# Kernel optimization log

Measured on AMD Instinct MI355X. Metric: run time of the kernel, lower is better.

## Reference

```python
import jax, jax.numpy as jnp
import numpy as np

HEADS = 8
DIM_HEAD = 64
C = 512              # in_channels == inner_dim = heads*dim_head
WIN = 7              # window size implied by rel_pos table (2*7-1 = 13)
EPS = 1e-5


def setup_inputs() -> dict:
    key = jax.random.key(0)
    ks = jax.random.split(key, 6)
    B = 2048
    inner = HEADS * DIM_HEAD
    x = jax.random.normal(ks[0], (B, C, WIN, WIN), dtype=jnp.float32)
    gamma = jnp.ones((C,), dtype=jnp.float32)
    beta = jnp.zeros((C,), dtype=jnp.float32)
    w_qkv = jax.random.normal(ks[1], (C, 3 * inner), dtype=jnp.float32) / np.sqrt(C)
    rel_table = jax.random.normal(ks[2], (2 * WIN - 1, 2 * WIN - 1, HEADS), dtype=jnp.float32)
    w_out = jax.random.normal(ks[3], (inner, C), dtype=jnp.float32) / np.sqrt(inner)
    b_out = jnp.zeros((C,), dtype=jnp.float32)
    return {"x": x, "gamma": gamma, "beta": beta, "w_qkv": w_qkv,
            "rel_table": rel_table, "w_out": w_out, "b_out": b_out}


def _rel_pos_bias(rel_table, H, W):
    # Swin-style additive bias: bias[h, i, j] = table[hi-hj+H-1, wi-wj+W-1, h]
    hh = jnp.arange(H)
    ww = jnp.arange(W)
    hi = jnp.repeat(hh, W)          # [N] row index of each flattened position
    wi = jnp.tile(ww, H)            # [N] col index
    dh = hi[:, None] - hi[None, :] + (H - 1)   # [N, N]
    dw = wi[:, None] - wi[None, :] + (W - 1)   # [N, N]
    bias = rel_table[dh, dw]        # [N, N, heads]
    return jnp.transpose(bias, (2, 0, 1))      # [heads, N, N]


def reference(x, gamma, beta, w_qkv, rel_table, w_out, b_out):
    B, Cc, H, W = x.shape
    N = H * W
    shortcut = x
    xs = jnp.transpose(x.reshape(B, Cc, N), (0, 2, 1))   # [B, N, C]
    # LayerNorm over channel dim
    mu = jnp.mean(xs, axis=-1, keepdims=True)
    var = jnp.var(xs, axis=-1, keepdims=True)
    xn = (xs - mu) * jax.lax.rsqrt(var + EPS) * gamma + beta
    qkv = xn @ w_qkv                                      # [B, N, 3*inner]
    q, k, v = jnp.split(qkv, 3, axis=-1)
    def heads(t):
        return jnp.transpose(t.reshape(B, N, HEADS, DIM_HEAD), (0, 2, 1, 3))  # [B,h,N,d]
    q, k, v = heads(q), heads(k), heads(v)
    scale = DIM_HEAD ** -0.5
    dots = jnp.einsum('bhnd,bhmd->bhnm', q, k) * scale   # [B,h,N,N]
    dots = dots + _rel_pos_bias(rel_table, H, W)[None]   # add Swin-style bias
    attn = jax.nn.softmax(dots, axis=-1)
    out = jnp.einsum('bhnm,bhmd->bhnd', attn, v)         # [B,h,N,d]
    out = jnp.transpose(out, (0, 2, 1, 3)).reshape(B, N, HEADS * DIM_HEAD)
    out = out @ w_out + b_out                            # [B, N, C]
    out = jnp.transpose(out, (0, 2, 1)).reshape(B, Cc, H, W)
    return out + shortcut
```

## Files before the change

kernel.cpp:

```cpp
#include <hip/hip_runtime.h>

#define BATCH 2048
#define CH 512
#define NTOK 49
#define NHEAD 8
#define DHEAD 64

typedef __attribute__((ext_vector_type(8))) short bf16x8;
typedef __attribute__((ext_vector_type(4))) float f32x4;

__device__ __forceinline__ ushort f2bf(float f) {
  union { float f; unsigned u; } v; v.f = f;
  unsigned r = v.u + 0x7fffu + ((v.u >> 16) & 1u);
  return (ushort)(r >> 16);
}

#define MFMA16(a, b, c) __builtin_amdgcn_mfma_f32_16x16x32_bf16((a), (b), (c), 0, 0, 0)

#define GLOAD_LDS16(gsrc, ldst)                                                  \
  __builtin_amdgcn_global_load_lds((const __attribute__((address_space(1))) void*)(gsrc), \
                                   (__attribute__((address_space(3))) void*)(ldst), 16, 0, 0)

__global__ void prep_kernel(const float* __restrict__ w_qkv, const float* __restrict__ w_out,
                            const float* __restrict__ rel, ushort* __restrict__ wqkvB,
                            ushort* __restrict__ woutF, float* __restrict__ biasP) {
  int tid = blockIdx.x * blockDim.x + threadIdx.x;
  int stride = gridDim.x * blockDim.x;
  for (int i = tid; i < 12 * 16 * 8 * 64 * 8; i += stride) {
    int j = i & 7, lane = (i >> 3) & 63, cbs = (i >> 9) & 7, kk = (i >> 12) & 15, nb = i >> 16;
    int o = nb * 128 + cbs * 16 + (lane & 15);
    int c = kk * 32 + (lane >> 4) * 8 + j;
    wqkvB[i] = f2bf(w_qkv[c * 1536 + o]);
  }
  for (int i = tid; i < 32 * 16 * 64 * 8; i += stride) {
    int j = i & 7, lane = (i >> 3) & 63, ks = (i >> 9) & 15, cb = i >> 13;
    int o = cb * 16 + (lane & 15);
    int c = ks * 32 + (lane >> 4) * 8 + j;
    woutF[i] = f2bf(w_out[c * 512 + o]);
  }
  for (int i = tid; i < NHEAD * 64 * 64; i += stride) {
    int h = i >> 12, n = (i >> 6) & 63, m = i & 63;
    float v = -1e30f;
    if (n < NTOK && m < NTOK) {
      int dh = n / 7 - m / 7 + 6;
      int dw = n % 7 - m % 7 + 6;
      v = rel[(dh * 13 + dw) * 8 + h];
    }
    biasP[i] = v;
  }
}

__global__ __launch_bounds__(256) void ln_kernel(const float* __restrict__ x,
                                                 const float* __restrict__ gamma,
                                                 const float* __restrict__ beta,
                                                 ushort* __restrict__ xnW) {
  int b = blockIdx.x;
  int t = threadIdx.x;
  __shared__ float xs[128][51];
  __shared__ float muL[64], rsL[64];
  const float* xb = x + (size_t)b * CH * NTOK;
  int row = t >> 2, sub = t & 3;
  float s = 0.f, s2 = 0.f;
  for (int cc = 0; cc < 4; cc++) {
    const float4* src4 = (const float4*)(xb + cc * 128 * NTOK);
    for (int i4 = t; i4 < 1568; i4 += 256) {
      float4 v = src4[i4];
      int lf = i4 * 4;
#pragma unroll
      for (int e = 0; e < 4; e++) {
        int c = (lf + e) / NTOK, n = (lf + e) - c * NTOK;
        xs[c][n] = ((const float*)&v)[e];
      }
    }
    __syncthreads();
    if (row < NTOK) {
      for (int c = sub; c < 128; c += 4) {
        float v = xs[c][row];
        s += v;
        s2 += v * v;
      }
    }
    __syncthreads();
  }
  s += __shfl_xor(s, 1);
  s += __shfl_xor(s, 2);
  s2 += __shfl_xor(s2, 1);
  s2 += __shfl_xor(s2, 2);
  if (sub == 0 && row < NTOK) {
    float m = s * (1.f / CH);
    muL[row] = m;
    rsL[row] = rsqrtf(s2 * (1.f / CH) - m * m + 1e-5f);
  }
  __syncthreads();
  ushort* dst = xnW + (size_t)b * NTOK * CH;
  for (int cc = 0; cc < 4; cc++) {
    const float4* src4 = (const float4*)(xb + cc * 128 * NTOK);
    for (int i4 = t; i4 < 1568; i4 += 256) {
      float4 v = src4[i4];
      int lf = i4 * 4;
#pragma unroll
      for (int e = 0; e < 4; e++) {
        int c = (lf + e) / NTOK, n = (lf + e) - c * NTOK;
        xs[c][n] = ((const float*)&v)[e];
      }
    }
    __syncthreads();
    for (int i = t; i < NTOK * 16; i += 256) {
      int n = i >> 4, c0 = (i & 15) * 8;
      ushort tmp[8];
#pragma unroll
      for (int j = 0; j < 8; j++) {
        int c = cc * 128 + c0 + j;
        tmp[j] = f2bf((xs[c0 + j][n] - muL[n]) * rsL[n] * gamma[c] + beta[c]);
      }
      *(uint4*)(dst + (size_t)n * CH + cc * 128 + c0) = *(const uint4*)tmp;
    }
    __syncthreads();
  }
}

__global__ __launch_bounds__(256, 4) void qkv_gemm(const ushort* __restrict__ xnW,
                                                   const ushort* __restrict__ wqkvB,
                                                   ushort* __restrict__ qW,
                                                   ushort* __restrict__ kW,
                                                   ushort* __restrict__ vW) {
  int bid = blockIdx.x;
  int f = (bid & 7) * 1536 + (bid >> 3);
  int mb = f / 12, nb = f - mb * 12;
  int b0 = mb * 2;
  int t = threadIdx.x, lane = t & 63, w = t >> 6;
  int wm = w >> 1, wn = w & 1;

  __shared__ __align__(16) ushort lds[16384];

  for (int i = t; i < 2 * 30 * 32; i += 256) {
    int buf = i >= 960;
    int r2 = i - buf * 960;
    int rr = r2 >> 5;
    int row = (rr < 15) ? (49 + rr) : (98 + rr);
    lds[buf * 8192 + row * 32 + (i & 31)] = 0;
  }

  const int arow = lane & 15, g = lane >> 4;
  int srow0 = w * 16 + (lane >> 2);
  int cL = lane & 3;
  const ushort* wBbase = wqkvB + (size_t)nb * 16 * 4096;

  {
#pragma unroll
    for (int i = 0; i < 2; i++) {
      int row = i * 64 + srow0;
      int n = row & 63, bb = b0 + (row >> 6);
      int cG = cL ^ ((row >> 1) & 3);
      if (n < NTOK)
        GLOAD_LDS16(xnW + ((size_t)bb * NTOK + n) * CH + cG * 8, lds + (i * 64 + w * 16) * 32);
    }
    GLOAD_LDS16(wBbase + (w * 2 + 0) * 512 + lane * 8, lds + 4096 + (w * 2 + 0) * 512);
    GLOAD_LDS16(wBbase + (w * 2 + 1) * 512 + lane * 8, lds + 4096 + (w * 2 + 1) * 512);
  }
  __syncthreads();

  f32x4 acc[4][4];
#pragma unroll
  for (int mt = 0; mt < 4; mt++)
#pragma unroll
    for (int nt = 0; nt < 4; nt++) acc[mt][nt] = (f32x4){0.f, 0.f, 0.f, 0.f};

  int cur = 0;
  for (int step = 0; step < 16; ++step) {
    if (step < 15) {
      int nxt = cur ^ 1, kk = step + 1;
#pragma unroll
      for (int i = 0; i < 2; i++) {
        int row = i * 64 + srow0;
        int n = row & 63, bb = b0 + (row >> 6);
        int cG = cL ^ ((row >> 1) & 3);
        if (n < NTOK)
          GLOAD_LDS16(xnW + ((size_t)bb * NTOK + n) * CH + kk * 32 + cG * 8,
                      lds + nxt * 8192 + (i * 64 + w * 16) * 32);
      }
      const ushort* wp = wBbase + (size_t)kk * 4096;
      GLOAD_LDS16(wp + (w * 2 + 0) * 512 + lane * 8, lds + nxt * 8192 + 4096 + (w * 2 + 0) * 512);
      GLOAD_LDS16(wp + (w * 2 + 1) * 512 + lane * 8, lds + nxt * 8192 + 4096 + (w * 2 + 1) * 512);
    }
    const ushort* lA = lds + cur * 8192;
    const ushort* lB = lds + cur * 8192 + 4096;
    bf16x8 bfr[4], afr[4];
#pragma unroll
    for (int nt = 0; nt < 4; nt++)
      bfr[nt] = *(const bf16x8*)&lB[((wn * 4 + nt) * 64 + lane) * 8];
#pragma unroll
    for (int mt = 0; mt < 4; mt++) {
      int row = wm * 64 + mt * 16 + arow;
      afr[mt] = *(const bf16x8*)&lA[row * 32 + (g ^ ((row >> 1) & 3)) * 8];
    }
#pragma unroll
    for (int mt = 0; mt < 4; mt++)
#pragma unroll
      for (int nt = 0; nt < 4; nt++) acc[mt][nt] = MFMA16(afr[mt], bfr[nt], acc[mt][nt]);
    __syncthreads();
    cur ^= 1;
  }

  ushort(*oL)[136] = (ushort(*)[136])lds;
  int h0 = (nb & 3) * 2;
  int sct = nb >> 2;
#pragma unroll
  for (int hh = 0; hh < 2; hh++) {
    if (wm == hh) {
#pragma unroll
      for (int mt = 0; mt < 4; mt++)
#pragma unroll
        for (int nt = 0; nt < 4; nt++)
#pragma unroll
          for (int r = 0; r < 4; r++) {
            int rn = mt * 16 + 4 * g + r;
            oL[rn][wn * 64 + nt * 16 + arow] = f2bf(acc[mt][nt][r]);
          }
    }
    __syncthreads();
    int b = b0 + hh;
    if (sct < 2) {
      ushort* dst = (sct == 0 ? qW : kW);
      for (int i = t; i < NTOK * 16; i += 256) {
        int n = i >> 4, c8 = i & 15;
        int h = h0 + (c8 >> 3);
        *(uint4*)(dst + (size_t)(b * 8 + h) * (NTOK * 64) + n * 64 + (c8 & 7) * 8) =
            *(const uint4*)&oL[n][c8 * 8];
      }
    } else {
      for (int i = t; i < 128 * 8; i += 256) {
        int col = i >> 3, n8 = i & 7;
        int h = h0 + (col >> 6), d = col & 63;
        ushort tmp[8];
#pragma unroll
        for (int jj = 0; jj < 8; jj++) tmp[jj] = oL[n8 * 8 + jj][col];
        *(uint4*)(vW + (size_t)(b * 8 + h) * 4096 + d * 64 + n8 * 8) = *(const uint4*)tmp;
      }
    }
    __syncthreads();
  }
}

__global__ __launch_bounds__(512, 4) void attn2(const ushort* __restrict__ qW,
                                                const ushort* __restrict__ kW,
                                                const ushort* __restrict__ vW,
                                                const float* __restrict__ biasP,
                                                ushort* __restrict__ aoW) {
  int b = blockIdx.x;
  int t = threadIdx.x;
  int lane = t & 63;
  int h = t >> 6;

  __shared__ ushort pL[8][64][72];
  ushort(*pl)[72] = pL[h];

  const int c = lane & 15, g = lane >> 4;
  const ushort* qb = qW + (size_t)(b * 8 + h) * NTOK * 64;
  const ushort* kb = kW + (size_t)(b * 8 + h) * NTOK * 64;
  const ushort* vb = vW + (size_t)(b * 8 + h) * 64 * 64;
  const float* bp = biasP + h * 64 * 64;

  f32x4 s[4][4];
#pragma unroll
  for (int mt = 0; mt < 4; mt++)
#pragma unroll
    for (int nt = 0; nt < 4; nt++) s[mt][nt] = (f32x4){0.f, 0.f, 0.f, 0.f};
#pragma unroll
  for (int ks = 0; ks < 2; ks++) {
    bf16x8 kf[4];
#pragma unroll
    for (int nt = 0; nt < 4; nt++)
      kf[nt] = *(const bf16x8*)(kb + (size_t)(nt * 16 + c) * 64 + ks * 32 + g * 8);
#pragma unroll
    for (int mt = 0; mt < 4; mt++) {
      bf16x8 qf = *(const bf16x8*)(qb + (size_t)(mt * 16 + c) * 64 + ks * 32 + g * 8);
#pragma unroll
      for (int nt = 0; nt < 4; nt++) s[mt][nt] = MFMA16(qf, kf[nt], s[mt][nt]);
    }
  }
#pragma unroll
  for (int mt = 0; mt < 4; mt++)
#pragma unroll
    for (int nt = 0; nt < 4; nt++)
#pragma unroll
      for (int r = 0; r < 4; r++) {
        int n = mt * 16 + 4 * g + r;
        int m = nt * 16 + c;
        s[mt][nt][r] = s[mt][nt][r] * 0.125f + bp[n * 64 + m];
      }

#pragma unroll
  for (int mt = 0; mt < 4; mt++)
#pragma unroll
    for (int r = 0; r < 4; r++) {
      float mx = fmaxf(fmaxf(s[mt][0][r], s[mt][1][r]), fmaxf(s[mt][2][r], s[mt][3][r]));
      mx = fmaxf(mx, __shfl_xor(mx, 1));
      mx = fmaxf(mx, __shfl_xor(mx, 2));
      mx = fmaxf(mx, __shfl_xor(mx, 4));
      mx = fmaxf(mx, __shfl_xor(mx, 8));
      float p0 = __expf(s[mt][0][r] - mx);
      float p1 = __expf(s[mt][1][r] - mx);
      float p2 = __expf(s[mt][2][r] - mx);
      float p3 = __expf(s[mt][3][r] - mx);
      float sum = p0 + p1 + p2 + p3;
      sum += __shfl_xor(sum, 1);
      sum += __shfl_xor(sum, 2);
      sum += __shfl_xor(sum, 4);
      sum += __shfl_xor(sum, 8);
      float rinv = 1.f / sum;
      int n = mt * 16 + 4 * g + r;
      pl[n][0 * 16 + c] = f2bf(p0 * rinv);
      pl[n][1 * 16 + c] = f2bf(p1 * rinv);
      pl[n][2 * 16 + c] = f2bf(p2 * rinv);
      pl[n][3 * 16 + c] = f2bf(p3 * rinv);
    }

  f32x4 o[4][4];
#pragma unroll
  for (int mt = 0; mt < 4; mt++)
#pragma unroll
    for (int nt = 0; nt < 4; nt++) o[mt][nt] = (f32x4){0.f, 0.f, 0.f, 0.f};
#pragma unroll
  for (int ks = 0; ks < 2; ks++) {
    bf16x8 vf[4];
#pragma unroll
    for (int nt = 0; nt < 4; nt++)
      vf[nt] = *(const bf16x8*)(vb + (size_t)(nt * 16 + c) * 64 + ks * 32 + g * 8);
#pragma unroll
    for (int mt = 0; mt < 4; mt++) {
      bf16x8 pf = *(const bf16x8*)&pl[mt * 16 + c][ks * 32 + g * 8];
#pragma unroll
      for (int nt = 0; nt < 4; nt++) o[mt][nt] = MFMA16(pf, vf[nt], o[mt][nt]);
    }
  }

#pragma unroll
  for (int mt = 0; mt < 4; mt++)
#pragma unroll
    for (int nt = 0; nt < 4; nt++)
#pragma unroll
      for (int r = 0; r < 4; r++) {
        int n = mt * 16 + 4 * g + r;
        pl[n][nt * 16 + c] = f2bf(o[mt][nt][r]);
      }
  ushort* ao = aoW + (size_t)b * NTOK * CH + h * 64;
  for (int i = lane; i < NTOK * 8; i += 64) {
    int row = i >> 3, c8 = i & 7;
    *(uint4*)(ao + (size_t)row * CH + c8 * 8) = *(const uint4*)&pl[row][c8 * 8];
  }
}

__global__ __launch_bounds__(256, 4) void proj_kernel(const ushort* __restrict__ aoW,
                                                      const ushort* __restrict__ woutF,
                                                      const float* __restrict__ b_out,
                                                      const float* __restrict__ x,
                                                      float* __restrict__ out) {
  int bid = blockIdx.x;
  int f = (bid & 7) * 512 + (bid >> 3);
  int mb = f >> 2, nbp = f & 3;
  int b0 = mb * 2;
  int t = threadIdx.x, lane = t & 63, w = t >> 6;
  int wm = w >> 1, wn = w & 1;

  __shared__ __align__(16) char ldsraw[33792];
  ushort* lds = (ushort*)ldsraw;
  float(*oL)[132] = (float(*)[132])ldsraw;

  for (int i = t; i < 2 * 30 * 32; i += 256) {
    int buf = i >= 960;
    int r2 = i - buf * 960;
    int rr = r2 >> 5;
    int row = (rr < 15) ? (49 + rr) : (98 + rr);
    lds[buf * 8192 + row * 32 + (i & 31)] = 0;
  }

  const int arow = lane & 15, g = lane >> 4;
  int srow0 = w * 16 + (lane >> 2);
  int cL = lane & 3;

  {
#pragma unroll
    for (int i = 0; i < 2; i++) {
      int row = i * 64 + srow0;
      int n = row & 63, bb = b0 + (row >> 6);
      int cG = cL ^ ((row >> 1) & 3);
      if (n < NTOK)
        GLOAD_LDS16(aoW + ((size_t)bb * NTOK + n) * CH + cG * 8, lds + (i * 64 + w * 16) * 32);
    }
    GLOAD_LDS16(woutF + ((size_t)(nbp * 8 + w * 2 + 0) * 16) * 512 + lane * 8,
                lds + 4096 + (w * 2 + 0) * 512);
    GLOAD_LDS16(woutF + ((size_t)(nbp * 8 + w * 2 + 1) * 16) * 512 + lane * 8,
                lds + 4096 + (w * 2 + 1) * 512);
  }
  __syncthreads();

  f32x4 acc[4][4];
#pragma unroll
  for (int mt = 0; mt < 4; mt++)
#pragma unroll
    for (int nt = 0; nt < 4; nt++) acc[mt][nt] = (f32x4){0.f, 0.f, 0.f, 0.f};

  int cur = 0;
  for (int step = 0; step < 16; ++step) {
    if (step < 15) {
      int nxt = cur ^ 1, kk = step + 1;
#pragma unroll
      for (int i = 0; i < 2; i++) {
        int row = i * 64 + srow0;
        int n = row & 63, bb = b0 + (row >> 6);
        int cG = cL ^ ((row >> 1) & 3);
        if (n < NTOK)
          GLOAD_LDS16(aoW + ((size_t)bb * NTOK + n) * CH + kk * 32 + cG * 8,
                      lds + nxt * 8192 + (i * 64 + w * 16) * 32);
      }
      GLOAD_LDS16(woutF + ((size_t)((nbp * 8 + w * 2 + 0) * 16 + kk)) * 512 + lane * 8,
                  lds + nxt * 8192 + 4096 + (w * 2 + 0) * 512);
      GLOAD_LDS16(woutF + ((size_t)((nbp * 8 + w * 2 + 1) * 16 + kk)) * 512 + lane * 8,
                  lds + nxt * 8192 + 4096 + (w * 2 + 1) * 512);
    }
    const ushort* lA = lds + cur * 8192;
    const ushort* lB = lds + cur * 8192 + 4096;
    bf16x8 bfr[4], afr[4];
#pragma unroll
    for (int nt = 0; nt < 4; nt++)
      bfr[nt] = *(const bf16x8*)&lB[((wn * 4 + nt) * 64 + lane) * 8];
#pragma unroll
    for (int mt = 0; mt < 4; mt++) {
      int row = wm * 64 + mt * 16 + arow;
      afr[mt] = *(const bf16x8*)&lA[row * 32 + (g ^ ((row >> 1) & 3)) * 8];
    }
#pragma unroll
    for (int mt = 0; mt < 4; mt++)
#pragma unroll
      for (int nt = 0; nt < 4; nt++) acc[mt][nt] = MFMA16(afr[mt], bfr[nt], acc[mt][nt]);
    __syncthreads();
    cur ^= 1;
  }

  const float* bo = b_out + nbp * 128;
#pragma unroll
  for (int hh = 0; hh < 2; hh++) {
    if (wm == hh) {
#pragma unroll
      for (int mt = 0; mt < 4; mt++)
#pragma unroll
        for (int nt = 0; nt < 4; nt++)
#pragma unroll
          for (int r = 0; r < 4; r++) {
            int rn = mt * 16 + 4 * g + r;
            if (rn < NTOK) oL[rn][wn * 64 + nt * 16 + arow] = acc[mt][nt][r];
          }
    }
    __syncthreads();
    int b = b0 + hh;
    const float4* x4 = (const float4*)(x + ((size_t)b * CH + nbp * 128) * NTOK);
    float4* o4 = (float4*)(out + ((size_t)b * CH + nbp * 128) * NTOK);
    for (int i = t; i < 1568; i += 256) {
      float4 xv = x4[i];
      float4 ov;
      int lf = i * 4;
#pragma unroll
      for (int e = 0; e < 4; e++) {
        int cl = (lf + e) / NTOK, n = (lf + e) - cl * NTOK;
        ((float*)&ov)[e] = oL[n][cl] + bo[cl] + ((const float*)&xv)[e];
      }
      o4[i] = ov;
    }
    __syncthreads();
  }
}

extern "C" void kernel_launch(void* const* d_in, const int* in_sizes, int n_in,
                              void* d_out, int out_size, void* d_ws, size_t ws_size,
                              hipStream_t stream) {
  const float* x = (const float*)d_in[0];
  const float* gamma = (const float*)d_in[1];
  const float* beta = (const float*)d_in[2];
  const float* w_qkv = (const float*)d_in[3];
  const float* rel = (const float*)d_in[4];
  const float* w_out = (const float*)d_in[5];
  const float* b_out = (const float*)d_in[6];
  float* out = (float*)d_out;

  char* ws = (char*)d_ws;
  size_t off = 0;
  ushort* wqkvB = (ushort*)(ws + off); off += (size_t)12 * 16 * 4096 * 2;
  ushort* woutF = (ushort*)(ws + off); off += (size_t)512 * 512 * 2;
  float* biasP = (float*)(ws + off);   off += (size_t)NHEAD * 64 * 64 * 4;
  ushort* qW = (ushort*)(ws + off);    off += ((size_t)BATCH * 8 * NTOK * 64 + 1024) * 2;
  ushort* kW = (ushort*)(ws + off);    off += ((size_t)BATCH * 8 * NTOK * 64 + 1024) * 2;
  ushort* vW = (ushort*)(ws + off);    off += (size_t)BATCH * 8 * 64 * 64 * 2;
  ushort* xnW = (ushort*)(ws + off);   off += (size_t)BATCH * NTOK * CH * 2;
  ushort* aoW = xnW;
  (void)ws_size;

  prep_kernel<<<1024, 256, 0, stream>>>(w_qkv, w_out, rel, wqkvB, woutF, biasP);
  ln_kernel<<<BATCH, 256, 0, stream>>>(x, gamma, beta, xnW);
  qkv_gemm<<<BATCH / 2 * 12, 256, 0, stream>>>(xnW, wqkvB, qW, kW, vW);
  attn2<<<BATCH, 512, 0, stream>>>(qW, kW, vW, biasP, aoW);
  proj_kernel<<<BATCH / 2 * 4, 256, 0, stream>>>(aoW, woutF, b_out, x, out);
}
```

Measured before the change: 663.6 us.

## Load GEMM weight fragments straight to registers; single-pass LayerNorm with bf16 LDS cache

The QKV and output-projection GEMMs now read the pre-shuffled weight fragments from global memory directly into registers each k-step, instead of staging them through LDS. This halves the LDS footprint per block (more blocks can be resident) and removes the LDS write/read for B. The trade-off is that weight loads are exposed in the loop without async prefetch. The LayerNorm kernel now reads x once into a bf16 LDS copy of the whole sample instead of reading it twice in float chunks. This halves global reads but normalises from bf16-rounded values, which costs some accuracy.

```diff
diff --git a/kernel.cpp b/kernel.cpp
--- a/kernel.cpp
+++ b/kernel.cpp
@@ -13,6 +13,11 @@
   union { float f; unsigned u; } v; v.f = f;
   unsigned r = v.u + 0x7fffu + ((v.u >> 16) & 1u);
   return (ushort)(r >> 16);
+}
+
+__device__ __forceinline__ float bf2f(ushort u) {
+  union { unsigned u; float f; } v; v.u = ((unsigned)u) << 16;
+  return v.f;
 }
 
 #define MFMA16(a, b, c) __builtin_amdgcn_mfma_f32_16x16x32_bf16((a), (b), (c), 0, 0, 0)
@@ -56,31 +61,28 @@
                                                  ushort* __restrict__ xnW) {
   int b = blockIdx.x;
   int t = threadIdx.x;
-  __shared__ float xs[128][51];
+  __shared__ ushort xsb[CH][NTOK];
   __shared__ float muL[64], rsL[64];
-  const float* xb = x + (size_t)b * CH * NTOK;
+  const float4* x4 = (const float4*)(x + (size_t)b * CH * NTOK);
+  for (int i4 = t; i4 < CH * NTOK / 4; i4 += 256) {
+    float4 v = x4[i4];
+    int lf = i4 * 4;
+#pragma unroll
+    for (int e = 0; e < 4; e++) {
+      int idx = lf + e;
+      int c = idx / NTOK, n = idx - c * NTOK;
+      xsb[c][n] = f2bf(((const float*)&v)[e]);
+    }
+  }
+  __syncthreads();
   int row = t >> 2, sub = t & 3;
   float s = 0.f, s2 = 0.f;
-  for (int cc = 0; cc < 4; cc++) {
-    const float4* src4 = (const float4*)(xb + cc * 128 * NTOK);
-    for (int i4 = t; i4 < 1568; i4 += 256) {
-      float4 v = src4[i4];
-      int lf = i4 * 4;
-#pragma unroll
-      for (int e = 0; e < 4; e++) {
-        int c = (lf + e) / NTOK, n = (lf + e) - c * NTOK;
-        xs[c][n] = ((const float*)&v)[e];
-      }
-    }
-    __syncthreads();
-    if (row < NTOK) {
-      for (int c = sub; c < 128; c += 4) {
-        float v = xs[c][row];
-        s += v;
-        s2 += v * v;
-      }
-    }
-    __syncthreads();
+  if (row < NTOK) {
+    for (int c = sub; c < CH; c += 4) {
+      float v = bf2f(xsb[c][row]);
+      s += v;
+      s2 += v * v;
+    }
   }
   s += __shfl_xor(s, 1);
   s += __shfl_xor(s, 2);
@@ -93,29 +95,16 @@
   }
   __syncthreads();
   ushort* dst = xnW + (size_t)b * NTOK * CH;
-  for (int cc = 0; cc < 4; cc++) {
-    const float4* src4 = (const float4*)(xb + cc * 128 * NTOK);
-    for (int i4 = t; i4 < 1568; i4 += 256) {
-      float4 v = src4[i4];
-      int lf = i4 * 4;
-#pragma unroll
-      for (int e = 0; e < 4; e++) {
-        int c = (lf + e) / NTOK, n = (lf + e) - c * NTOK;
-        xs[c][n] = ((const float*)&v)[e];
-      }
-    }
-    __syncthreads();
-    for (int i = t; i < NTOK * 16; i += 256) {
-      int n = i >> 4, c0 = (i & 15) * 8;
-      ushort tmp[8];
-#pragma unroll
-      for (int j = 0; j < 8; j++) {
-        int c = cc * 128 + c0 + j;
-        tmp[j] = f2bf((xs[c0 + j][n] - muL[n]) * rsL[n] * gamma[c] + beta[c]);
-      }
-      *(uint4*)(dst + (size_t)n * CH + cc * 128 + c0) = *(const uint4*)tmp;
-    }
-    __syncthreads();
+  for (int i = t; i < NTOK * 64; i += 256) {
+    int n = i >> 6, c0 = (i & 63) * 8;
+    float mu = muL[n], rs = rsL[n];
+    ushort tmp[8];
+#pragma unroll
+    for (int j = 0; j < 8; j++) {
+      int c = c0 + j;
+      tmp[j] = f2bf((bf2f(xsb[c][n]) - mu) * rs * gamma[c] + beta[c]);
+    }
+    *(uint4*)(dst + (size_t)n * CH + c0) = *(const uint4*)tmp;
   }
 }
 
@@ -131,14 +120,14 @@
   int t = threadIdx.x, lane = t & 63, w = t >> 6;
   int wm = w >> 1, wn = w & 1;
 
-  __shared__ __align__(16) ushort lds[16384];
+  __shared__ __align__(16) ushort lds[8704];
 
   for (int i = t; i < 2 * 30 * 32; i += 256) {
     int buf = i >= 960;
     int r2 = i - buf * 960;
     int rr = r2 >> 5;
     int row = (rr < 15) ? (49 + rr) : (98 + rr);
-    lds[buf * 8192 + row * 32 + (i & 31)] = 0;
+    lds[buf * 4096 + row * 32 + (i & 31)] = 0;
   }
 
   const int arow = lane & 15, g = lane >> 4;
@@ -155,8 +144,6 @@
       if (n < NTOK)
         GLOAD_LDS16(xnW + ((size_t)bb * NTOK + n) * CH + cG * 8, lds + (i * 64 + w * 16) * 32);
     }
-    GLOAD_LDS16(wBbase + (w * 2 + 0) * 512 + lane * 8, lds + 4096 + (w * 2 + 0) * 512);
-    GLOAD_LDS16(wBbase + (w * 2 + 1) * 512 + lane * 8, lds + 4096 + (w * 2 + 1) * 512);
   }
   __syncthreads();
 
@@ -168,6 +155,10 @@
 
   int cur = 0;
   for (int step = 0; step < 16; ++step) {
+    const ushort* wp = wBbase + (size_t)step * 4096 + (wn * 4) * 512 + lane * 8;
+    bf16x8 bfr[4];
+#pragma unroll
+    for (int nt = 0; nt < 4; nt++) bfr[nt] = *(const bf16x8*)(wp + nt * 512);
     if (step < 15) {
       int nxt = cur ^ 1, kk = step + 1;
 #pragma unroll
@@ -177,18 +168,11 @@
         int cG = cL ^ ((row >> 1) & 3);
         if (n < NTOK)
           GLOAD_LDS16(xnW + ((size_t)bb * NTOK + n) * CH + kk * 32 + cG * 8,
-                      lds + nxt * 8192 + (i * 64 + w * 16) * 32);
-      }
-      const ushort* wp = wBbase + (size_t)kk * 4096;
-      GLOAD_LDS16(wp + (w * 2 + 0) * 512 + lane * 8, lds + nxt * 8192 + 4096 + (w * 2 + 0) * 512);
-      GLOAD_LDS16(wp + (w * 2 + 1) * 512 + lane * 8, lds + nxt * 8192 + 4096 + (w * 2 + 1) * 512);
-    }
-    const ushort* lA = lds + cur * 8192;
-    const ushort* lB = lds + cur * 8192 + 4096;
-    bf16x8 bfr[4], afr[4];
-#pragma unroll
-    for (int nt = 0; nt < 4; nt++)
-      bfr[nt] = *(const bf16x8*)&lB[((wn * 4 + nt) * 64 + lane) * 8];
+                      lds + nxt * 4096 + (i * 64 + w * 16) * 32);
+      }
+    }
+    const ushort* lA = lds + cur * 4096;
+    bf16x8 afr[4];
 #pragma unroll
     for (int mt = 0; mt < 4; mt++) {
       int row = wm * 64 + mt * 16 + arow;
@@ -372,7 +356,7 @@
     int r2 = i - buf * 960;
     int rr = r2 >> 5;
     int row = (rr < 15) ? (49 + rr) : (98 + rr);
-    lds[buf * 8192 + row * 32 + (i & 31)] = 0;
+    lds[buf * 4096 + row * 32 + (i & 31)] = 0;
   }
 
   const int arow = lane & 15, g = lane >> 4;
@@ -388,10 +372,6 @@
       if (n < NTOK)
         GLOAD_LDS16(aoW + ((size_t)bb * NTOK + n) * CH + cG * 8, lds + (i * 64 + w * 16) * 32);
     }
-    GLOAD_LDS16(woutF + ((size_t)(nbp * 8 + w * 2 + 0) * 16) * 512 + lane * 8,
-                lds + 4096 + (w * 2 + 0) * 512);
-    GLOAD_LDS16(woutF + ((size_t)(nbp * 8 + w * 2 + 1) * 16) * 512 + lane * 8,
-                lds + 4096 + (w * 2 + 1) * 512);
   }
   __syncthreads();
 
@@ -403,6 +383,10 @@
 
   int cur = 0;
   for (int step = 0; step < 16; ++step) {
+    const ushort* wp = woutF + ((size_t)(nbp * 8 + wn * 4) * 16 + step) * 512 + lane * 8;
+    bf16x8 bfr[4];
+#pragma unroll
+    for (int nt = 0; nt < 4; nt++) bfr[nt] = *(const bf16x8*)(wp + (size_t)nt * 16 * 512);
     if (step < 15) {
       int nxt = cur ^ 1, kk = step + 1;
 #pragma unroll
@@ -412,19 +396,11 @@
         int cG = cL ^ ((row >> 1) & 3);
         if (n < NTOK)
           GLOAD_LDS16(aoW + ((size_t)bb * NTOK + n) * CH + kk * 32 + cG * 8,
-                      lds + nxt * 8192 + (i * 64 + w * 16) * 32);
-      }
-      GLOAD_LDS16(woutF + ((size_t)((nbp * 8 + w * 2 + 0) * 16 + kk)) * 512 + lane * 8,
-                  lds + nxt * 8192 + 4096 + (w * 2 + 0) * 512);
-      GLOAD_LDS16(woutF + ((size_t)((nbp * 8 + w * 2 + 1) * 16 + kk)) * 512 + lane * 8,
-                  lds + nxt * 8192 + 4096 + (w * 2 + 1) * 512);
-    }
-    const ushort* lA = lds + cur * 8192;
-    const ushort* lB = lds + cur * 8192 + 4096;
-    bf16x8 bfr[4], afr[4];
-#pragma unroll
-    for (int nt = 0; nt < 4; nt++)
-      bfr[nt] = *(const bf16x8*)&lB[((wn * 4 + nt) * 64 + lane) * 8];
+                      lds + nxt * 4096 + (i * 64 + w * 16) * 32);
+      }
+    }
+    const ushort* lA = lds + cur * 4096;
+    bf16x8 afr[4];
 #pragma unroll
     for (int mt = 0; mt < 4; mt++) {
       int row = wm * 64 + mt * 16 + arow;
```

Result: faster. 640.6 us (-3.5%).
